# Performance work log

Measured on AMD Instinct MI355X. Metric: run time of the kernel, lower is better.

The kernel has to match this reference:

```python
import jax, jax.numpy as jnp
import numpy as np


def setup_inputs() -> dict:
    key = jax.random.key(0)
    ks = jax.random.split(key, 6)
    T, B, N = 2048, 32, 1024
    return {
        "decoder_hx": jax.random.normal(ks[0], (B, N), dtype=jnp.float32),
        "encoder_outputs": jax.random.normal(ks[1], (T, B, N), dtype=jnp.float32),
        "encoder_feature": jax.random.normal(ks[2], (T, B, N), dtype=jnp.float32),
        "mask_tensor": jnp.ones((B, T), dtype=jnp.float32),
        "Ws_w": jax.random.normal(ks[3], (N, N), dtype=jnp.float32) / np.sqrt(N),
        "Ws_b": jnp.zeros((N,), dtype=jnp.float32),
        "v_w": jax.random.normal(ks[4], (1, N), dtype=jnp.float32) / np.sqrt(N),
        "v_b": jnp.zeros((1,), dtype=jnp.float32),
        "lin_w": jax.random.normal(ks[5], (N, 2 * N), dtype=jnp.float32) / np.sqrt(2 * N),
        "lin_b": jnp.zeros((N,), dtype=jnp.float32),
    }


def reference(decoder_hx, encoder_outputs, encoder_feature, mask_tensor,
              Ws_w, Ws_b, v_w, v_b, lin_w, lin_b):
    # Bahdanau additive attention.
    # dec_feature = W_s(decoder_hx): (b, n), broadcast over time t_k
    dec_feature = decoder_hx @ Ws_w.T + Ws_b                     # (b, n)
    e = jnp.tanh(encoder_feature + dec_feature[None, :, :])      # (t, b, n)
    # scores = v(e): rank-1 projection to a scalar per (t, b)
    scores = jnp.einsum('tbn,n->bt', e, v_w[0]) + v_b[0]         # (b, t)
    attn_dist = jax.nn.softmax(scores, axis=1) * mask_tensor     # (b, t)
    # weighted temporal sum of encoder outputs -> context vector
    content_vector = jnp.einsum('bt,tbn->bn', attn_dist, encoder_outputs)
    concat = jnp.concatenate([content_vector, decoder_hx], axis=1)  # (b, 2n)
    hx_attention = jnp.tanh(concat @ lin_w.T + lin_b)            # (b, n)
    return hx_attention
```

## Files before the change

### kernel.cpp

```cpp
#include <hip/hip_runtime.h>
#include <math.h>

#define T 2048
#define B 32
#define N 1024
#define NCHUNK 64
#define TCHUNK (T / NCHUNK)

__device__ __forceinline__ float fast_tanh(float x) {
    float e = __expf(2.0f * x);
    return 1.0f - 2.0f * __builtin_amdgcn_rcpf(e + 1.0f);
}

__device__ __forceinline__ float wave_reduce_sum(float v) {
    #pragma unroll
    for (int off = 32; off > 0; off >>= 1) v += __shfl_down(v, off, 64);
    return v;
}

__global__ void dec_feature_kernel(const float* __restrict__ hx,
                                   const float* __restrict__ Ws_w,
                                   const float* __restrict__ Ws_b,
                                   float* __restrict__ dec) {
    int w = blockIdx.x * 4 + (threadIdx.x >> 6);
    int lane = threadIdx.x & 63;
    int i = w >> 5;
    int b = w & 31;
    const float4* wr = (const float4*)(Ws_w + (size_t)i * N);
    const float4* hr = (const float4*)(hx + (size_t)b * N);
    float acc = 0.f;
    #pragma unroll
    for (int k = 0; k < 4; ++k) {
        float4 a = wr[k * 64 + lane];
        float4 h = hr[k * 64 + lane];
        acc += a.x * h.x + a.y * h.y + a.z * h.z + a.w * h.w;
    }
    acc = wave_reduce_sum(acc);
    if (lane == 0) dec[(size_t)b * N + i] = acc + Ws_b[i];
}

__global__ void scores_kernel(const float* __restrict__ ef,
                              const float* __restrict__ dec,
                              const float* __restrict__ v_w,
                              const float* __restrict__ v_b,
                              float* __restrict__ scores) {
    int w = blockIdx.x * 4 + (threadIdx.x >> 6);
    int lane = threadIdx.x & 63;
    int t = w >> 5;
    int b = w & 31;
    const float4* e4 = (const float4*)(ef + (size_t)w * N);
    const float4* d4 = (const float4*)(dec + (size_t)b * N);
    const float4* v4 = (const float4*)v_w;
    float acc = 0.f;
    #pragma unroll
    for (int k = 0; k < 4; ++k) {
        float4 e = e4[k * 64 + lane];
        float4 d = d4[k * 64 + lane];
        float4 v = v4[k * 64 + lane];
        acc += fast_tanh(e.x + d.x) * v.x + fast_tanh(e.y + d.y) * v.y
             + fast_tanh(e.z + d.z) * v.z + fast_tanh(e.w + d.w) * v.w;
    }
    acc = wave_reduce_sum(acc);
    if (lane == 0) scores[(size_t)b * T + t] = acc + v_b[0];
}

__global__ void softmax_kernel(const float* __restrict__ scores,
                               const float* __restrict__ mask,
                               float* __restrict__ attn) {
    int b = blockIdx.x;
    int tid = threadIdx.x;
    int lane = tid & 63, wid = tid >> 6;
    float s[8];
    float m = -1e30f;
    #pragma unroll
    for (int k = 0; k < 8; ++k) {
        s[k] = scores[(size_t)b * T + tid + k * 256];
        m = fmaxf(m, s[k]);
    }
    __shared__ float redm[4], reds[4];
    #pragma unroll
    for (int off = 32; off > 0; off >>= 1) m = fmaxf(m, __shfl_down(m, off, 64));
    if (lane == 0) redm[wid] = m;
    __syncthreads();
    m = fmaxf(fmaxf(redm[0], redm[1]), fmaxf(redm[2], redm[3]));
    float sum = 0.f;
    #pragma unroll
    for (int k = 0; k < 8; ++k) { s[k] = __expf(s[k] - m); sum += s[k]; }
    sum = wave_reduce_sum(sum);
    if (lane == 0) reds[wid] = sum;
    __syncthreads();
    float inv = __builtin_amdgcn_rcpf(reds[0] + reds[1] + reds[2] + reds[3]);
    #pragma unroll
    for (int k = 0; k < 8; ++k)
        attn[(size_t)b * T + tid + k * 256] =
            s[k] * inv * mask[(size_t)b * T + tid + k * 256];
}

__global__ void content_partial_kernel(const float* __restrict__ eo,
                                       const float* __restrict__ attn,
                                       float* __restrict__ partial) {
    int b = blockIdx.y;
    int chunk = blockIdx.x;
    int tid = threadIdx.x;
    const float4* base = (const float4*)eo;
    float4 acc = {0.f, 0.f, 0.f, 0.f};
    #pragma unroll 4
    for (int tt = 0; tt < TCHUNK; ++tt) {
        int t = chunk * TCHUNK + tt;
        float a = attn[(size_t)b * T + t];
        float4 e = base[((size_t)t * B + b) * (N / 4) + tid];
        acc.x += a * e.x; acc.y += a * e.y; acc.z += a * e.z; acc.w += a * e.w;
    }
    ((float4*)partial)[((size_t)chunk * B + b) * (N / 4) + tid] = acc;
}

__global__ void content_reduce_kernel(const float* __restrict__ partial,
                                      float* __restrict__ content) {
    int g = blockIdx.x * 256 + threadIdx.x;
    const float4* p4 = (const float4*)partial;
    float4 acc = {0.f, 0.f, 0.f, 0.f};
    #pragma unroll 8
    for (int c = 0; c < NCHUNK; ++c) {
        float4 v = p4[(size_t)c * (B * N / 4) + g];
        acc.x += v.x; acc.y += v.y; acc.z += v.z; acc.w += v.w;
    }
    ((float4*)content)[g] = acc;
}

__global__ void out_kernel(const float* __restrict__ content,
                           const float* __restrict__ hx,
                           const float* __restrict__ lin_w,
                           const float* __restrict__ lin_b,
                           float* __restrict__ out) {
    int w = blockIdx.x * 4 + (threadIdx.x >> 6);
    int lane = threadIdx.x & 63;
    int i = w >> 5;
    int b = w & 31;
    const float4* wr = (const float4*)(lin_w + (size_t)i * 2 * N);
    const float4* cr = (const float4*)(content + (size_t)b * N);
    const float4* hr = (const float4*)(hx + (size_t)b * N);
    float acc = 0.f;
    #pragma unroll
    for (int k = 0; k < 4; ++k) {
        float4 a = wr[k * 64 + lane];
        float4 c = cr[k * 64 + lane];
        acc += a.x * c.x + a.y * c.y + a.z * c.z + a.w * c.w;
    }
    #pragma unroll
    for (int k = 0; k < 4; ++k) {
        float4 a = wr[256 + k * 64 + lane];
        float4 h = hr[k * 64 + lane];
        acc += a.x * h.x + a.y * h.y + a.z * h.z + a.w * h.w;
    }
    acc = wave_reduce_sum(acc);
    if (lane == 0) out[(size_t)b * N + i] = fast_tanh(acc + lin_b[i]);
}

extern "C" void kernel_launch(void* const* d_in, const int* in_sizes, int n_in,
                              void* d_out, int out_size, void* d_ws, size_t ws_size,
                              hipStream_t stream) {
    const float* hx    = (const float*)d_in[0];
    const float* eo    = (const float*)d_in[1];
    const float* ef    = (const float*)d_in[2];
    const float* mask  = (const float*)d_in[3];
    const float* Ws_w  = (const float*)d_in[4];
    const float* Ws_b  = (const float*)d_in[5];
    const float* v_w   = (const float*)d_in[6];
    const float* v_b   = (const float*)d_in[7];
    const float* lin_w = (const float*)d_in[8];
    const float* lin_b = (const float*)d_in[9];
    float* out = (float*)d_out;

    float* ws      = (float*)d_ws;
    float* dec     = ws;
    float* scores  = dec + B * N;
    float* attn    = scores + B * T;
    float* content = attn + B * T;
    float* partial = content + B * N;

    dec_feature_kernel<<<(B * N) / 4, 256, 0, stream>>>(hx, Ws_w, Ws_b, dec);
    scores_kernel<<<(T * B) / 4, 256, 0, stream>>>(ef, dec, v_w, v_b, scores);
    softmax_kernel<<<B, 256, 0, stream>>>(scores, mask, attn);
    content_partial_kernel<<<dim3(NCHUNK, B), 256, 0, stream>>>(eo, attn, partial);
    content_reduce_kernel<<<(B * N / 4) / 256, 256, 0, stream>>>(partial, content);
    out_kernel<<<(B * N) / 4, 256, 0, stream>>>(content, hx, lin_w, lin_b, out);
}
```

Measured before the change: 563.8 us.

## Fuse softmax into content partial kernel and halve time chunks

```diff
diff --git a/kernel.cpp b/kernel.cpp
--- a/kernel.cpp
+++ b/kernel.cpp
@@ -4,7 +4,7 @@
 #define T 2048
 #define B 32
 #define N 1024
-#define NCHUNK 64
+#define NCHUNK 32
 #define TCHUNK (T / NCHUNK)
 
 __device__ __forceinline__ float fast_tanh(float x) {
@@ -44,11 +44,13 @@
                               const float* __restrict__ v_w,
                               const float* __restrict__ v_b,
                               float* __restrict__ scores) {
-    int w = blockIdx.x * 4 + (threadIdx.x >> 6);
+    int bx = blockIdx.x;
+    int b = bx & 31;
+    int tq = bx >> 5;
+    int wid = threadIdx.x >> 6;
     int lane = threadIdx.x & 63;
-    int t = w >> 5;
-    int b = w & 31;
-    const float4* e4 = (const float4*)(ef + (size_t)w * N);
+    int t = tq * 4 + wid;
+    const float4* e4 = (const float4*)(ef + ((size_t)t * B + b) * N);
     const float4* d4 = (const float4*)(dec + (size_t)b * N);
     const float4* v4 = (const float4*)v_w;
     float acc = 0.f;
@@ -64,12 +66,17 @@
     if (lane == 0) scores[(size_t)b * T + t] = acc + v_b[0];
 }
 
-__global__ void softmax_kernel(const float* __restrict__ scores,
-                               const float* __restrict__ mask,
-                               float* __restrict__ attn) {
-    int b = blockIdx.x;
+__global__ void content_partial_kernel(const float* __restrict__ eo,
+                                       const float* __restrict__ scores,
+                                       const float* __restrict__ mask,
+                                       float* __restrict__ partial) {
+    int b = blockIdx.y;
+    int chunk = blockIdx.x;
     int tid = threadIdx.x;
     int lane = tid & 63, wid = tid >> 6;
+    __shared__ float red[4];
+    __shared__ float p_sh[TCHUNK];
+
     float s[8];
     float m = -1e30f;
     #pragma unroll
@@ -77,37 +84,34 @@
         s[k] = scores[(size_t)b * T + tid + k * 256];
         m = fmaxf(m, s[k]);
     }
-    __shared__ float redm[4], reds[4];
     #pragma unroll
     for (int off = 32; off > 0; off >>= 1) m = fmaxf(m, __shfl_down(m, off, 64));
-    if (lane == 0) redm[wid] = m;
+    if (lane == 0) red[wid] = m;
     __syncthreads();
-    m = fmaxf(fmaxf(redm[0], redm[1]), fmaxf(redm[2], redm[3]));
+    m = fmaxf(fmaxf(red[0], red[1]), fmaxf(red[2], red[3]));
+    __syncthreads();
+
     float sum = 0.f;
     #pragma unroll
-    for (int k = 0; k < 8; ++k) { s[k] = __expf(s[k] - m); sum += s[k]; }
+    for (int k = 0; k < 8; ++k) sum += __expf(s[k] - m);
     sum = wave_reduce_sum(sum);
-    if (lane == 0) reds[wid] = sum;
+    if (lane == 0) red[wid] = sum;
     __syncthreads();
-    float inv = __builtin_amdgcn_rcpf(reds[0] + reds[1] + reds[2] + reds[3]);
-    #pragma unroll
-    for (int k = 0; k < 8; ++k)
-        attn[(size_t)b * T + tid + k * 256] =
-            s[k] * inv * mask[(size_t)b * T + tid + k * 256];
-}
+    float invL = __builtin_amdgcn_rcpf(red[0] + red[1] + red[2] + red[3]);
 
-__global__ void content_partial_kernel(const float* __restrict__ eo,
-                                       const float* __restrict__ attn,
-                                       float* __restrict__ partial) {
-    int b = blockIdx.y;
-    int chunk = blockIdx.x;
-    int tid = threadIdx.x;
+    if (tid < TCHUNK) {
+        int t = chunk * TCHUNK + tid;
+        p_sh[tid] = __expf(scores[(size_t)b * T + t] - m) * invL
+                  * mask[(size_t)b * T + t];
+    }
+    __syncthreads();
+
     const float4* base = (const float4*)eo;
     float4 acc = {0.f, 0.f, 0.f, 0.f};
     #pragma unroll 4
     for (int tt = 0; tt < TCHUNK; ++tt) {
         int t = chunk * TCHUNK + tt;
-        float a = attn[(size_t)b * T + t];
+        float a = p_sh[tt];
         float4 e = base[((size_t)t * B + b) * (N / 4) + tid];
         acc.x += a * e.x; acc.y += a * e.y; acc.z += a * e.z; acc.w += a * e.w;
     }
@@ -174,14 +178,12 @@
     float* ws      = (float*)d_ws;
     float* dec     = ws;
     float* scores  = dec + B * N;
-    float* attn    = scores + B * T;
-    float* content = attn + B * T;
+    float* content = scores + B * T;
     float* partial = content + B * N;
 
     dec_feature_kernel<<<(B * N) / 4, 256, 0, stream>>>(hx, Ws_w, Ws_b, dec);
     scores_kernel<<<(T * B) / 4, 256, 0, stream>>>(ef, dec, v_w, v_b, scores);
-    softmax_kernel<<<B, 256, 0, stream>>>(scores, mask, attn);
-    content_partial_kernel<<<dim3(NCHUNK, B), 256, 0, stream>>>(eo, attn, partial);
+    content_partial_kernel<<<dim3(NCHUNK, B), 256, 0, stream>>>(eo, scores, mask, partial);
     content_reduce_kernel<<<(B * N / 4) / 256, 256, 0, stream>>>(partial, content);
     out_kernel<<<(B * N) / 4, 256, 0, stream>>>(content, hx, lin_w, lin_b, out);
 }
```

Measured after the change: 554.3 us. No clear change (-1.7%).
